# Performance work log

Hardware: AMD Instinct MI355X
Metric: run time of the kernel (lower is better)

The kernel has to match this reference:

```python
import jax, jax.numpy as jnp
import numpy as np

B, S, D, K = 4, 2048, 1024, 8

def setup_inputs() -> dict:
    key = jax.random.key(0)
    k1, k2, k3 = jax.random.split(key, 3)
    hidden_states = jax.random.normal(k1, (B, S, D), dtype=jnp.float32)
    # scaled so scores ~ O(1) and exp() does not overflow
    W_phi = jax.random.normal(k2, (D, D), dtype=jnp.float32) * 0.005
    W_psi = jax.random.normal(k3, (D, D), dtype=jnp.float32) * 0.005
    return {"hidden_states": hidden_states, "W_phi": W_phi, "W_psi": W_psi, "k": K}

def reference(hidden_states, W_phi, W_psi, k):
    b, s, d = hidden_states.shape
    k = min(k, s)
    # nn.Linear(bias=False): y = x @ W.T
    phi_h = hidden_states @ W_phi.T            # [b,s,d]
    psi_h = hidden_states @ W_psi.T            # [b,s,d]
    scores = jnp.einsum('bsd,btd->bst', phi_h, psi_h)  # [b,s,s]
    affinity = jnp.exp(scores)
    topk_values, topk_indices = jax.lax.top_k(affinity, k)   # [b,s,k]
    norm_sum = topk_values.sum(axis=-1, keepdims=True) + 1e-8
    normalized_weights = topk_values / norm_sum
    batch_offset = (jnp.arange(b) * s)[:, None, None]        # [b,1,1]
    src_local = jnp.arange(s)[None, :, None]                 # [1,s,1]
    src_global = jnp.broadcast_to(batch_offset + src_local, (b, s, k))
    dst_global = batch_offset + topk_indices
    mask = (topk_indices != src_local).reshape(-1)           # drop self-loops
    # eager boolean compaction (data-dependent size, like the torch module)
    src_final = src_global.reshape(-1)[mask]
    dst_final = dst_global.reshape(-1)[mask]
    weights_final = normalized_weights.reshape(-1)[mask]
    if src_final.size == 0:
        all_nodes = jnp.arange(b * s)
        return jnp.stack([all_nodes, all_nodes], axis=0), jnp.ones(b * s, dtype=jnp.float32)
    edge_index = jnp.stack([src_final, dst_final], axis=0)
    return edge_index, weights_final
```

## Files before the change

kernel.cpp:

```cpp
#include <hip/hip_runtime.h>
#include <cmath>

#define SEQ 2048
#define DDIM 1024
#define NROWS 8192
#define KSEL 8
#define IMAXC 0x7fffffff

typedef __attribute__((ext_vector_type(8))) short bf16x8;
typedef __attribute__((ext_vector_type(4))) float f32x4;
typedef __attribute__((ext_vector_type(4))) double f64x4;

__device__ __forceinline__ unsigned short f2bf(float f) {
  unsigned u = __builtin_bit_cast(unsigned, f);
  u = (u + 0x7fffu + ((u >> 16) & 1u)) >> 16;
  return (unsigned short)u;
}
__device__ __forceinline__ float bf2f(unsigned short h) {
  unsigned u = ((unsigned)h) << 16;
  return __builtin_bit_cast(float, u);
}
__device__ __forceinline__ unsigned pkbf(float a, float b) {
  unsigned r;
  asm("v_cvt_pk_bf16_f32 %0, %1, %2" : "=v"(r) : "v"(a), "v"(b));
  return r;
}
__device__ __forceinline__ void dmap(int sel, int lg, int lr, int rg,
                                     int& ri, int& ci) {
  switch (sel) {
    case 0:  ri = (lg << 2) + rg; ci = lr; break;
    case 1:  ri = lg + (rg << 2); ci = lr; break;
    case 2:  ri = lr; ci = (lg << 2) + rg; break;
    default: ri = lr; ci = lg + (rg << 2); break;
  }
}

__global__ void kprobe(int* __restrict__ sel) {
  const int lane = threadIdx.x;
  const int lr = lane & 15, lg = lane >> 4;
  const double a = (double)(4 * lr + lg + 1);
  const double b = (double)(9 * lr + 5 * lg + 2);
  f64x4 d = (f64x4){0.0, 0.0, 0.0, 0.0};
  d = __builtin_amdgcn_mfma_f64_16x16x4f64(a, b, d, 0, 0, 0);
  int my = 4;
  for (int s = 3; s >= 0; --s) {
    bool ok = true;
    for (int rg = 0; rg < 4; ++rg) {
      int ri, ci;
      dmap(s, lg, lr, rg, ri, ci);
      double e = 0.0;
      for (int k = 0; k < 4; ++k)
        e += (double)(4 * ri + k + 1) * (double)(9 * ci + 5 * k + 2);
      ok = ok && (d[rg] == e);
    }
    if (__all(ok)) my = s;
  }
  if (lane == 0) sel[0] = my;
}

__global__ __launch_bounds__(256, 2)
void k0_mfma(const float* __restrict__ A, const float* __restrict__ B,
             float* __restrict__ C, const int* __restrict__ selp) {
  const int sel = selp[0];
  if (sel >= 4) return;
  __shared__ float As[32][72];
  __shared__ float Bs[32][72];
  const int tid = threadIdx.x;
  const int lane = tid & 63, w = tid >> 6;
  const int wr = w >> 1, wc = w & 1;
  const int lr = lane & 15, lg = lane >> 4;
  const int brow = blockIdx.y << 6, bcol = blockIdx.x << 6;
  const int kr = tid >> 3, c4 = (tid & 7) << 2;

  f64x4 acc[2][2];
#pragma unroll
  for (int mi = 0; mi < 2; ++mi)
#pragma unroll
    for (int nj = 0; nj < 2; ++nj)
      acc[mi][nj] = (f64x4){0.0, 0.0, 0.0, 0.0};

  const float* Ap = &A[(size_t)kr * DDIM + brow + c4];
  const float* Bp = &B[(size_t)kr * DDIM + bcol + c4];
  float4 pa0 = *reinterpret_cast<const float4*>(Ap);
  float4 pa1 = *reinterpret_cast<const float4*>(Ap + 32);
  float4 pb0 = *reinterpret_cast<const float4*>(Bp);
  float4 pb1 = *reinterpret_cast<const float4*>(Bp + 32);

  for (int k0 = 0; k0 < DDIM; k0 += 32) {
    __syncthreads();
    *reinterpret_cast<float4*>(&As[kr][c4]) = pa0;
    *reinterpret_cast<float4*>(&As[kr][c4 + 32]) = pa1;
    *reinterpret_cast<float4*>(&Bs[kr][c4]) = pb0;
    *reinterpret_cast<float4*>(&Bs[kr][c4 + 32]) = pb1;
    __syncthreads();
    if (k0 + 32 < DDIM) {
      const size_t nk = (size_t)(k0 + 32) * DDIM;
      pa0 = *reinterpret_cast<const float4*>(Ap + nk);
      pa1 = *reinterpret_cast<const float4*>(Ap + nk + 32);
      pb0 = *reinterpret_cast<const float4*>(Bp + nk);
      pb1 = *reinterpret_cast<const float4*>(Bp + nk + 32);
    }
#pragma unroll
    for (int kp = 0; kp < 8; ++kp) {
      const int ka = (kp << 2) + lg;
      double a[2], b[2];
#pragma unroll
      for (int mi = 0; mi < 2; ++mi)
        a[mi] = (double)As[ka][(wr << 5) + (mi << 4) + lr];
#pragma unroll
      for (int nj = 0; nj < 2; ++nj)
        b[nj] = (double)Bs[ka][(wc << 5) + (nj << 4) + lr];
#pragma unroll
      for (int mi = 0; mi < 2; ++mi)
#pragma unroll
        for (int nj = 0; nj < 2; ++nj)
          acc[mi][nj] = __builtin_amdgcn_mfma_f64_16x16x4f64(
              a[mi], b[nj], acc[mi][nj], 0, 0, 0);
    }
  }
#pragma unroll
  for (int mi = 0; mi < 2; ++mi)
#pragma unroll
    for (int nj = 0; nj < 2; ++nj)
#pragma unroll
      for (int rg = 0; rg < 4; ++rg) {
        int ri, ci;
        dmap(sel, lg, lr, rg, ri, ci);
        C[(size_t)(brow + (wr << 5) + (mi << 4) + ri) * DDIM +
          bcol + (wc << 5) + (nj << 4) + ci] = (float)acc[mi][nj][rg];
      }
}

__global__ __launch_bounds__(256)
void k0_repair(const float* __restrict__ A, const float* __restrict__ B,
               float* __restrict__ C, const int* __restrict__ selp) {
  if (selp[0] < 4) return;
  __shared__ __align__(16) float As[32][68];
  __shared__ __align__(16) float Bs[32][68];
  const int tid = threadIdx.x;
  const int tx = tid & 15, ty = tid >> 4;
  const int brow = blockIdx.y << 6;
  const int bcol = blockIdx.x << 6;
  double acc[4][4] = {};
  for (int k0 = 0; k0 < DDIM; k0 += 32) {
#pragma unroll
    for (int i = 0; i < 2; ++i) {
      const int f = tid + (i << 8);
      const int r = f >> 4;
      const int c4 = (f & 15) << 2;
      *reinterpret_cast<float4*>(&As[r][c4]) =
          *reinterpret_cast<const float4*>(&A[(size_t)(k0 + r) * DDIM + brow + c4]);
      *reinterpret_cast<float4*>(&Bs[r][c4]) =
          *reinterpret_cast<const float4*>(&B[(size_t)(k0 + r) * DDIM + bcol + c4]);
    }
    __syncthreads();
#pragma unroll
    for (int kk = 0; kk < 32; ++kk) {
      const float4 a = *reinterpret_cast<const float4*>(&As[kk][ty << 2]);
      const float4 b = *reinterpret_cast<const float4*>(&Bs[kk][tx << 2]);
      const double ad[4] = {a.x, a.y, a.z, a.w};
      const double bd[4] = {b.x, b.y, b.z, b.w};
#pragma unroll
      for (int i = 0; i < 4; ++i)
#pragma unroll
        for (int j = 0; j < 4; ++j)
          acc[i][j] = fma(ad[i], bd[j], acc[i][j]);
    }
    __syncthreads();
  }
#pragma unroll
  for (int i = 0; i < 4; ++i) {
    float4 v = make_float4((float)acc[i][0], (float)acc[i][1],
                           (float)acc[i][2], (float)acc[i][3]);
    *reinterpret_cast<float4*>(
        &C[(size_t)(brow + (ty << 2) + i) * DDIM + bcol + (tx << 2)]) = v;
  }
}

#define K1_STAGE(bi)                                              \
  do {                                                            \
    As[bi][akh + 0][ar] = pa0.x; As[bi][akh + 1][ar] = pa0.y;     \
    As[bi][akh + 2][ar] = pa0.z; As[bi][akh + 3][ar] = pa0.w;     \
    As[bi][akh + 4][ar] = pa1.x; As[bi][akh + 5][ar] = pa1.y;     \
    As[bi][akh + 6][ar] = pa1.z; As[bi][akh + 7][ar] = pa1.w;     \
    *reinterpret_cast<float4*>(&Bs[bi][bk][bc4]) = pb0;           \
    *reinterpret_cast<float4*>(&Bs[bi][bk][bc4 + 64]) = pb1;      \
  } while (0)

__global__ __launch_bounds__(256, 2)
void k1_mfma(const float* __restrict__ A, const float* __restrict__ B,
             float* __restrict__ C, const int* __restrict__ selp) {
  const int sel = selp[0];
  if (sel >= 4) return;
  __shared__ float As[2][16][144];
  __shared__ float Bs[2][16][144];
  const int tid = threadIdx.x;
  const int lin = blockIdx.y * 8 + blockIdx.x;
  const int nlin = (lin & 7) * 64 + (lin >> 3);
  const int brow = (nlin >> 3) << 7;
  const int bcol = (nlin & 7) << 7;
  const int lane = tid & 63, w = tid >> 6;
  const int wr = w >> 1, wc = w & 1;
  const int lr = lane & 15, lg = lane >> 4;
  const int ar = tid >> 1, akh = (tid & 1) << 3;
  const int bk = tid >> 4, bc4 = (tid & 15) << 2;

  f64x4 acc[4][4];
#pragma unroll
  for (int mi = 0; mi < 4; ++mi)
#pragma unroll
    for (int nj = 0; nj < 4; ++nj)
      acc[mi][nj] = (f64x4){0.0, 0.0, 0.0, 0.0};

  const float* Ap = &A[(size_t)(brow + ar) * DDIM + akh];
  const float* Bp = &B[(size_t)bk * DDIM + bcol + bc4];

  float4 pa0 = *reinterpret_cast<const float4*>(Ap);
  float4 pa1 = *reinterpret_cast<const float4*>(Ap + 4);
  float4 pb0 = *reinterpret_cast<const float4*>(Bp);
  float4 pb1 = *reinterpret_cast<const float4*>(Bp + 64);
  K1_STAGE(0);
  pa0 = *reinterpret_cast<const float4*>(Ap + 16);
  pa1 = *reinterpret_cast<const float4*>(Ap + 20);
  pb0 = *reinterpret_cast<const float4*>(Bp + (size_t)16 * DDIM);
  pb1 = *reinterpret_cast<const float4*>(Bp + (size_t)16 * DDIM + 64);

  for (int t = 0; t < 64; ++t) {
    __syncthreads();
    const int cur = t & 1;
    if (t < 63) {
      K1_STAGE(cur ^ 1);
      if (t < 62) {
        const size_t ko = (size_t)(t + 2) << 4;
        pa0 = *reinterpret_cast<const float4*>(Ap + ko);
        pa1 = *reinterpret_cast<const float4*>(Ap + ko + 4);
        pb0 = *reinterpret_cast<const float4*>(Bp + ko * DDIM);
        pb1 = *reinterpret_cast<const float4*>(Bp + ko * DDIM + 64);
      }
    }
#pragma unroll
    for (int kp = 0; kp < 4; ++kp) {
      const int ka = (kp << 2) + lg;
      double a[4], b[4];
#pragma unroll
      for (int mi = 0; mi < 4; ++mi)
        a[mi] = (double)As[cur][ka][(wr << 6) + (mi << 4) + lr];
#pragma unroll
      for (int nj = 0; nj < 4; ++nj)
        b[nj] = (double)Bs[cur][ka][(wc << 6) + (nj << 4) + lr];
#pragma unroll
      for (int mi = 0; mi < 4; ++mi)
#pragma unroll
        for (int nj = 0; nj < 4; ++nj)
          acc[mi][nj] = __builtin_amdgcn_mfma_f64_16x16x4f64(
              a[mi], b[nj], acc[mi][nj], 0, 0, 0);
    }
  }
#pragma unroll
  for (int mi = 0; mi < 4; ++mi)
#pragma unroll
    for (int nj = 0; nj < 4; ++nj)
#pragma unroll
      for (int rg = 0; rg < 4; ++rg) {
        int ri, ci;
        dmap(sel, lg, lr, rg, ri, ci);
        C[(size_t)(brow + (wr << 6) + (mi << 4) + ri) * DDIM +
          bcol + (wc << 6) + (nj << 4) + ci] = (float)acc[mi][nj][rg];
      }
}

__global__ __launch_bounds__(256, 2)
void k1_repair(const float* __restrict__ A, const float* __restrict__ B,
               float* __restrict__ C, const int* __restrict__ selp) {
  if (selp[0] < 4) return;
  __shared__ double As[128][17];
  __shared__ double Bs[16][130];
  const int tid = threadIdx.x;
  const int lin = blockIdx.y * 8 + blockIdx.x;
  const int nlin = (lin & 7) * 64 + (lin >> 3);
  const int brow = (nlin >> 3) << 7;
  const int bcol = (nlin & 7) << 7;
  const int tx = tid & 15, ty = tid >> 4;
  const int ar = tid >> 1, aks = (tid & 1) << 3;
  const int bk = tid >> 4, btx = tid & 15;

  double acc[8][8];
#pragma unroll
  for (int i = 0; i < 8; ++i)
#pragma unroll
    for (int j = 0; j < 8; ++j) acc[i][j] = 0.0;

  const float* Aptr = &A[(size_t)(brow + ar) * DDIM + aks];
  const float* Bptr = &B[(size_t)bk * DDIM + bcol + (btx << 1)];

  float4 pa0, pa1;
  float2 pb[4];
  pa0 = *reinterpret_cast<const float4*>(Aptr);
  pa1 = *reinterpret_cast<const float4*>(Aptr + 4);
#pragma unroll
  for (int w = 0; w < 4; ++w)
    pb[w] = *reinterpret_cast<const float2*>(Bptr + (w << 5));

  for (int k0 = 0; k0 < DDIM; k0 += 16) {
    __syncthreads();
    As[ar][aks + 0] = (double)pa0.x; As[ar][aks + 1] = (double)pa0.y;
    As[ar][aks + 2] = (double)pa0.z; As[ar][aks + 3] = (double)pa0.w;
    As[ar][aks + 4] = (double)pa1.x; As[ar][aks + 5] = (double)pa1.y;
    As[ar][aks + 6] = (double)pa1.z; As[ar][aks + 7] = (double)pa1.w;
#pragma unroll
    for (int w = 0; w < 4; ++w) {
      Bs[bk][(btx << 1) + (w << 5) + 0] = (double)pb[w].x;
      Bs[bk][(btx << 1) + (w << 5) + 1] = (double)pb[w].y;
    }
    __syncthreads();
    if (k0 + 16 < DDIM) {
      pa0 = *reinterpret_cast<const float4*>(Aptr + k0 + 16);
      pa1 = *reinterpret_cast<const float4*>(Aptr + k0 + 20);
#pragma unroll
      for (int w = 0; w < 4; ++w)
        pb[w] = *reinterpret_cast<const float2*>(
            Bptr + (size_t)(k0 + 16) * DDIM + (w << 5));
    }
#pragma unroll 8
    for (int kk = 0; kk < 16; ++kk) {
      double a[8];
      double2 b[4];
#pragma unroll
      for (int i = 0; i < 8; ++i) a[i] = As[(ty << 3) + i][kk];
#pragma unroll
      for (int jj = 0; jj < 4; ++jj)
        b[jj] = *reinterpret_cast<const double2*>(&Bs[kk][(tx << 1) + (jj << 5)]);
#pragma unroll
      for (int i = 0; i < 8; ++i) {
#pragma unroll
        for (int jj = 0; jj < 4; ++jj) {
          acc[i][(jj << 1) + 0] = fma(a[i], b[jj].x, acc[i][(jj << 1) + 0]);
          acc[i][(jj << 1) + 1] = fma(a[i], b[jj].y, acc[i][(jj << 1) + 1]);
        }
      }
    }
  }
#pragma unroll
  for (int i = 0; i < 8; ++i) {
    float* crow = &C[(size_t)(brow + (ty << 3) + i) * DDIM + bcol + (tx << 1)];
#pragma unroll
    for (int jj = 0; jj < 4; ++jj) {
      float2 v = make_float2((float)acc[i][(jj << 1)],
                             (float)acc[i][(jj << 1) + 1]);
      *reinterpret_cast<float2*>(crow + (jj << 5)) = v;
    }
  }
}

__global__ __launch_bounds__(512, 1)
void k2_mfma(const float* __restrict__ T, const float* __restrict__ H,
             unsigned short* __restrict__ cand_v,
             unsigned char* __restrict__ cand_i) {
  __shared__ union {
    unsigned short stage[2][256 * 64];
    float Sl[64][264];
    struct {
      float mv[512][8];
      unsigned char mi[512][8];
    } mg;
  } u;
  const int tid = threadIdx.x;
  const int lane = tid & 63;
  const int w = tid >> 6;
  const int wr = w >> 2, wc = w & 3;
  const int lr = lane & 15, lg = lane >> 4;
  const int z = blockIdx.z;
  const int bx = blockIdx.x;
  const int brow = blockIdx.y << 8, bcol = bx << 8;
  const int row0g = z * SEQ + brow;
  const int col0g = z * SEQ + bcol;

  f32x4 acc[8][4];
#pragma unroll
  for (int mi = 0; mi < 8; ++mi)
#pragma unroll
    for (int nj = 0; nj < 4; ++nj)
      acc[mi][nj] = (f32x4){0.f, 0.f, 0.f, 0.f};

  for (int k0 = 0; k0 < DDIM; k0 += 64) {
    __syncthreads();
#pragma unroll
    for (int q = 0; q < 4; ++q) {
      const int c = (q << 9) + tid;
      const int row = c >> 3, slot = c & 7;
      const int gs = slot ^ (row & 7);
      {
        const float* s = &T[(size_t)(row0g + row) * DDIM + k0 + (gs << 3)];
        const float4 f0 = *reinterpret_cast<const float4*>(s);
        const float4 f1 = *reinterpret_cast<const float4*>(s + 4);
        uint4 o;
        o.x = pkbf(f0.x, f0.y); o.y = pkbf(f0.z, f0.w);
        o.z = pkbf(f1.x, f1.y); o.w = pkbf(f1.z, f1.w);
        *reinterpret_cast<uint4*>(&u.stage[0][c << 3]) = o;
      }
      {
        const float* s = &H[(size_t)(col0g + row) * DDIM + k0 + (gs << 3)];
        const float4 f0 = *reinterpret_cast<const float4*>(s);
        const float4 f1 = *reinterpret_cast<const float4*>(s + 4);
        uint4 o;
        o.x = pkbf(f0.x, f0.y); o.y = pkbf(f0.z, f0.w);
        o.z = pkbf(f1.x, f1.y); o.w = pkbf(f1.z, f1.w);
        *reinterpret_cast<uint4*>(&u.stage[1][c << 3]) = o;
      }
    }
    __syncthreads();
#pragma unroll
    for (int kh = 0; kh < 2; ++kh) {
      const int sl = (kh << 2) + lg;
      bf16x8 bfv[4];
#pragma unroll
      for (int nj = 0; nj < 4; ++nj) {
        const int rb = (wc << 6) + (nj << 4) + lr;
        bfv[nj] = *reinterpret_cast<const bf16x8*>(
            &u.stage[1][(rb << 6) + ((sl ^ (rb & 7)) << 3)]);
      }
#pragma unroll
      for (int mi = 0; mi < 8; ++mi) {
        const int ra = (wr << 7) + (mi << 4) + lr;
        const bf16x8 af = *reinterpret_cast<const bf16x8*>(
            &u.stage[0][(ra << 6) + ((sl ^ (ra & 7)) << 3)]);
#pragma unroll
        for (int nj = 0; nj < 4; ++nj)
          acc[mi][nj] = __builtin_amdgcn_mfma_f32_16x16x32_bf16(
              af, bfv[nj], acc[mi][nj], 0, 0, 0);
      }
    }
  }

  const int srow = tid >> 3;
  const int qd = tid & 7;
#pragma unroll
  for (int p = 0; p < 4; ++p) {
    __syncthreads();
    if (wr == (p >> 1)) {
      const int mib = (p & 1) << 2;
#pragma unroll
      for (int mi2 = 0; mi2 < 4; ++mi2)
#pragma unroll
        for (int nj = 0; nj < 4; ++nj)
#pragma unroll
          for (int rg = 0; rg < 4; ++rg)
            u.Sl[(mi2 << 4) + (lg << 2) + rg][(wc << 6) + (nj << 4) + lr] =
                acc[mib + mi2][nj][rg];
    }
    __syncthreads();
    float v[KSEL];
    int ci[KSEL];
#pragma unroll
    for (int s = 0; s < KSEL; ++s) { v[s] = -3.0e38f; ci[s] = 0; }
    const int c0 = qd << 5;
    for (int c = 0; c < 32; ++c) {
      const float x = u.Sl[srow][c0 + c];
      if (x > v[KSEL - 1]) {
        float pv = x; int pc = c0 + c;
#pragma unroll
        for (int s = 0; s < KSEL; ++s) {
          if (x > v[s]) {
            const float tv = v[s]; const int tc = ci[s];
            v[s] = pv; ci[s] = pc; pv = tv; pc = tc;
          }
        }
      }
    }
    __syncthreads();
#pragma unroll
    for (int s = 0; s < KSEL; ++s) {
      u.mg.mv[tid][s] = v[s];
      u.mg.mi[tid][s] = (unsigned char)ci[s];
    }
    __syncthreads();
    if (qd == 0) {
      float fv[KSEL];
      int fi[KSEL];
#pragma unroll
      for (int s = 0; s < KSEL; ++s) { fv[s] = -3.0e38f; fi[s] = 0; }
#pragma unroll
      for (int t = 0; t < 8; ++t) {
#pragma unroll
        for (int s = 0; s < KSEL; ++s) {
          const float x = u.mg.mv[tid + t][s];
          const int idx = u.mg.mi[tid + t][s];
          if (x > fv[KSEL - 1]) {
            float pv = x; int pc = idx;
#pragma unroll
            for (int s2 = 0; s2 < KSEL; ++s2) {
              if (x > fv[s2]) {
                const float tv = fv[s2]; const int tc = fi[s2];
                fv[s2] = pv; fi[s2] = pc; pv = tv; pc = tc;
              }
            }
          }
        }
      }
      const size_t base =
          (size_t)(row0g + (p << 6) + srow) * 64 + ((size_t)bx << 3);
#pragma unroll
      for (int s = 0; s < KSEL; ++s) {
        cand_v[base + s] = f2bf(fv[s]);
        cand_i[base + s] = (unsigned char)fi[s];
      }
    }
  }
}

__global__ __launch_bounds__(256)
void kr_rescore(const float* __restrict__ T, const float* __restrict__ H,
                const unsigned short* __restrict__ cand_v,
                const unsigned char* __restrict__ cand_i,
                int* __restrict__ topi, float* __restrict__ topw,
                int* __restrict__ cnt) {
  const int tid = threadIdx.x, lane = tid & 63, w = tid >> 6;
  const int r = blockIdx.x * 4 + w;
  const int b = r >> 11, iloc = r & (SEQ - 1);

  const size_t cbase = (size_t)r * 64;
  float v0 = bf2f(cand_v[cbase + lane]);
  int i0 = ((lane >> 3) << 8) + cand_i[cbase + lane];
  int keep = 0;
  for (int rnd = 0; rnd < 16; ++rnd) {
    float m = v0;
#pragma unroll
    for (int off = 32; off >= 1; off >>= 1) m = fmaxf(m, __shfl_xor(m, off));
    const unsigned long long bm = __ballot(v0 == m);
    const int owner = __ffsll(bm) - 1;
    const int oi = __shfl(i0, owner);
    if (lane == owner) v0 = -3.0e38f;
    if (lane == rnd) keep = oi;
  }

  const float* Trow = T + (size_t)r * DDIM;
  float4 t4[4];
#pragma unroll
  for (int q = 0; q < 4; ++q)
    t4[q] = *reinterpret_cast<const float4*>(&Trow[(q << 8) + (lane << 2)]);

  float t8v[KSEL];
  int t8i[KSEL];
#pragma unroll
  for (int p = 0; p < KSEL; ++p) { t8v[p] = -1.0f; t8i[p] = IMAXC; }

  for (int c = 0; c < 16; ++c) {
    const int j = __shfl(keep, c);
    const float* Hrow = H + ((size_t)(b << 11) + j) * DDIM;
    double s = 0.0;
#pragma unroll
    for (int q = 0; q < 4; ++q) {
      const float4 h = *reinterpret_cast<const float4*>(&Hrow[(q << 8) + (lane << 2)]);
      s = fma((double)t4[q].x, (double)h.x, s);
      s = fma((double)t4[q].y, (double)h.y, s);
      s = fma((double)t4[q].z, (double)h.z, s);
      s = fma((double)t4[q].w, (double)h.w, s);
    }
#pragma unroll
    for (int off = 1; off < 64; off <<= 1) s += __shfl_xor(s, off);
    const float aff = expf((float)s);
    const bool g7 = (aff > t8v[KSEL - 1]) ||
                    (aff == t8v[KSEL - 1] && j < t8i[KSEL - 1]);
    if (g7) {
      float pv = aff; int pi = j;
#pragma unroll
      for (int p = 0; p < KSEL; ++p) {
        const bool g = (aff > t8v[p]) || (aff == t8v[p] && j < t8i[p]);
        if (g) {
          const float tv = t8v[p]; const int ti = t8i[p];
          t8v[p] = pv; t8i[p] = pi; pv = tv; pi = ti;
        }
      }
    }
  }
  if (lane == 0) {
    float sum = 0.0f;
#pragma unroll
    for (int p = 0; p < KSEL; ++p) sum += t8v[p];
    sum += 1e-8f;
    int c8 = KSEL;
#pragma unroll
    for (int p = 0; p < KSEL; ++p)
      if (t8i[p] == iloc) --c8;
    cnt[r] = c8;
#pragma unroll
    for (int p = 0; p < KSEL; ++p) {
      topi[(size_t)r * KSEL + p] = t8i[p];
      topw[(size_t)r * KSEL + p] = t8v[p] / sum;
    }
  }
}

__global__ __launch_bounds__(1024)
void k4_scan(const int* __restrict__ cnt, int* __restrict__ off) {
  __shared__ int part[1024];
  const int t = threadIdx.x;
  int loc[8];
  int s = 0;
#pragma unroll
  for (int i = 0; i < 8; ++i) { loc[i] = s; s += cnt[t * 8 + i]; }
  part[t] = s;
  __syncthreads();
  for (int d = 1; d < 1024; d <<= 1) {
    const int add = (t >= d) ? part[t - d] : 0;
    __syncthreads();
    part[t] += add;
    __syncthreads();
  }
  const int base = (t == 0) ? 0 : part[t - 1];
#pragma unroll
  for (int i = 0; i < 8; ++i) off[t * 8 + i] = base + loc[i];
}

__global__ __launch_bounds__(256)
void k5_emit(const int* __restrict__ topi, const float* __restrict__ topw,
             const int* __restrict__ off, float* __restrict__ out, int E) {
  const int r = blockIdx.x * 256 + threadIdx.x;
  if (r >= NROWS) return;
  const int o = off[r];
  const int sloc = r & (SEQ - 1);
  const int bbase = r & ~(SEQ - 1);
  int e = 0;
#pragma unroll
  for (int p = 0; p < KSEL; ++p) {
    const int id = topi[(size_t)r * KSEL + p];
    const float w = topw[(size_t)r * KSEL + p];
    if (id != sloc) {
      const int pos = o + e;
      if (pos < E) {
        out[pos] = (float)r;
        out[(size_t)E + pos] = (float)(bbase + id);
        out[2 * (size_t)E + pos] = w;
      }
      ++e;
    }
  }
}

extern "C" void kernel_launch(void* const* d_in, const int* in_sizes, int n_in,
                              void* d_out, int out_size, void* d_ws,
                              size_t ws_size, hipStream_t stream) {
  const float* H = (const float*)d_in[0];
  const float* Wphi = (const float*)d_in[1];
  const float* Wpsi = (const float*)d_in[2];
  float* out = (float*)d_out;
  const int E = out_size / 3;

  char* base = (char*)d_ws;
  float* T = (float*)base;
  char* regionX = base + 33554432;
  float* Wc = (float*)regionX;
  unsigned short* cand_v = (unsigned short*)regionX;
  unsigned char* cand_i = (unsigned char*)(regionX + 2097152);
  char* pp = regionX + 4194304;
  int* topi = (int*)pp;  pp += 262144;
  float* topw = (float*)pp; pp += 262144;
  int* cnt = (int*)pp;   pp += 32768;
  int* off = (int*)pp;   pp += 32768;
  int* sel = (int*)pp;

  kprobe<<<dim3(1), 64, 0, stream>>>(sel);
  k0_mfma<<<dim3(16, 16), 256, 0, stream>>>(Wphi, Wpsi, Wc, sel);
  k0_repair<<<dim3(16, 16), 256, 0, stream>>>(Wphi, Wpsi, Wc, sel);
  k1_mfma<<<dim3(8, 64), 256, 0, stream>>>(H, Wc, T, sel);
  k1_repair<<<dim3(8, 64), 256, 0, stream>>>(H, Wc, T, sel);
  k2_mfma<<<dim3(8, 8, 4), 512, 0, stream>>>(T, H, cand_v, cand_i);
  kr_rescore<<<dim3(NROWS / 4), 256, 0, stream>>>(T, H, cand_v, cand_i,
                                                  topi, topw, cnt);
  k4_scan<<<dim3(1), 1024, 0, stream>>>(cnt, off);
  k5_emit<<<dim3(NROWS / 256), 256, 0, stream>>>(topi, topw, off, out, E);
}
```

Before: 592.1 us.

## Double-buffer LDS staging in k0 and k2 GEMMs and raise MFMA wave priority

New measurement: 563.0 us. 1.05x faster.

```diff
diff --git a/kernel.cpp b/kernel.cpp
--- a/kernel.cpp
+++ b/kernel.cpp
@@ -58,13 +58,21 @@
   if (lane == 0) sel[0] = my;
 }
 
+#define K0_STAGE(bi)                                        \
+  do {                                                      \
+    *reinterpret_cast<float4*>(&As[bi][kr][c4]) = pa0;      \
+    *reinterpret_cast<float4*>(&As[bi][kr][c4 + 32]) = pa1; \
+    *reinterpret_cast<float4*>(&Bs[bi][kr][c4]) = pb0;      \
+    *reinterpret_cast<float4*>(&Bs[bi][kr][c4 + 32]) = pb1; \
+  } while (0)
+
 __global__ __launch_bounds__(256, 2)
 void k0_mfma(const float* __restrict__ A, const float* __restrict__ B,
              float* __restrict__ C, const int* __restrict__ selp) {
   const int sel = selp[0];
   if (sel >= 4) return;
-  __shared__ float As[32][72];
-  __shared__ float Bs[32][72];
+  __shared__ float As[2][32][72];
+  __shared__ float Bs[2][32][72];
   const int tid = threadIdx.x;
   const int lane = tid & 63, w = tid >> 6;
   const int wr = w >> 1, wc = w & 1;
@@ -85,31 +93,39 @@
   float4 pa1 = *reinterpret_cast<const float4*>(Ap + 32);
   float4 pb0 = *reinterpret_cast<const float4*>(Bp);
   float4 pb1 = *reinterpret_cast<const float4*>(Bp + 32);
-
-  for (int k0 = 0; k0 < DDIM; k0 += 32) {
-    __syncthreads();
-    *reinterpret_cast<float4*>(&As[kr][c4]) = pa0;
-    *reinterpret_cast<float4*>(&As[kr][c4 + 32]) = pa1;
-    *reinterpret_cast<float4*>(&Bs[kr][c4]) = pb0;
-    *reinterpret_cast<float4*>(&Bs[kr][c4 + 32]) = pb1;
-    __syncthreads();
-    if (k0 + 32 < DDIM) {
-      const size_t nk = (size_t)(k0 + 32) * DDIM;
-      pa0 = *reinterpret_cast<const float4*>(Ap + nk);
-      pa1 = *reinterpret_cast<const float4*>(Ap + nk + 32);
-      pb0 = *reinterpret_cast<const float4*>(Bp + nk);
-      pb1 = *reinterpret_cast<const float4*>(Bp + nk + 32);
-    }
+  K0_STAGE(0);
+  {
+    const size_t nk = (size_t)32 * DDIM;
+    pa0 = *reinterpret_cast<const float4*>(Ap + nk);
+    pa1 = *reinterpret_cast<const float4*>(Ap + nk + 32);
+    pb0 = *reinterpret_cast<const float4*>(Bp + nk);
+    pb1 = *reinterpret_cast<const float4*>(Bp + nk + 32);
+  }
+
+  for (int t = 0; t < 32; ++t) {
+    __syncthreads();
+    const int cur = t & 1;
+    if (t < 31) {
+      K0_STAGE(cur ^ 1);
+      if (t < 30) {
+        const size_t nk = (size_t)(t + 2) * 32 * DDIM;
+        pa0 = *reinterpret_cast<const float4*>(Ap + nk);
+        pa1 = *reinterpret_cast<const float4*>(Ap + nk + 32);
+        pb0 = *reinterpret_cast<const float4*>(Bp + nk);
+        pb1 = *reinterpret_cast<const float4*>(Bp + nk + 32);
+      }
+    }
+    __builtin_amdgcn_s_setprio(1);
 #pragma unroll
     for (int kp = 0; kp < 8; ++kp) {
       const int ka = (kp << 2) + lg;
       double a[2], b[2];
 #pragma unroll
       for (int mi = 0; mi < 2; ++mi)
-        a[mi] = (double)As[ka][(wr << 5) + (mi << 4) + lr];
+        a[mi] = (double)As[cur][ka][(wr << 5) + (mi << 4) + lr];
 #pragma unroll
       for (int nj = 0; nj < 2; ++nj)
-        b[nj] = (double)Bs[ka][(wc << 5) + (nj << 4) + lr];
+        b[nj] = (double)Bs[cur][ka][(wc << 5) + (nj << 4) + lr];
 #pragma unroll
       for (int mi = 0; mi < 2; ++mi)
 #pragma unroll
@@ -117,6 +133,7 @@
           acc[mi][nj] = __builtin_amdgcn_mfma_f64_16x16x4f64(
               a[mi], b[nj], acc[mi][nj], 0, 0, 0);
     }
+    __builtin_amdgcn_s_setprio(0);
   }
 #pragma unroll
   for (int mi = 0; mi < 2; ++mi)
@@ -238,6 +255,7 @@
         pb1 = *reinterpret_cast<const float4*>(Bp + ko * DDIM + 64);
       }
     }
+    __builtin_amdgcn_s_setprio(1);
 #pragma unroll
     for (int kp = 0; kp < 4; ++kp) {
       const int ka = (kp << 2) + lg;
@@ -255,6 +273,7 @@
           acc[mi][nj] = __builtin_amdgcn_mfma_f64_16x16x4f64(
               a[mi], b[nj], acc[mi][nj], 0, 0, 0);
     }
+    __builtin_amdgcn_s_setprio(0);
   }
 #pragma unroll
   for (int mi = 0; mi < 4; ++mi)
@@ -352,12 +371,48 @@
   }
 }
 
+#define K2_LOAD(koff)                                                         \
+  do {                                                                        \
+    _Pragma("unroll")                                                         \
+    for (int q = 0; q < 4; ++q) {                                             \
+      const int c = (q << 9) + tid;                                           \
+      const int row = c >> 3;                                                 \
+      const int gs = (c & 7) ^ (row & 7);                                     \
+      const float* sT = &T[(size_t)(row0g + row) * DDIM + (koff) + (gs << 3)];\
+      rT[2 * q] = *reinterpret_cast<const float4*>(sT);                       \
+      rT[2 * q + 1] = *reinterpret_cast<const float4*>(sT + 4);               \
+      const float* sH = &H[(size_t)(col0g + row) * DDIM + (koff) + (gs << 3)];\
+      rH[2 * q] = *reinterpret_cast<const float4*>(sH);                       \
+      rH[2 * q + 1] = *reinterpret_cast<const float4*>(sH + 4);               \
+    }                                                                         \
+  } while (0)
+
+#define K2_STAGE(bi)                                                          \
+  do {                                                                        \
+    _Pragma("unroll")                                                         \
+    for (int q = 0; q < 4; ++q) {                                             \
+      const int c = (q << 9) + tid;                                           \
+      uint4 o;                                                                \
+      o.x = pkbf(rT[2 * q].x, rT[2 * q].y);                                   \
+      o.y = pkbf(rT[2 * q].z, rT[2 * q].w);                                   \
+      o.z = pkbf(rT[2 * q + 1].x, rT[2 * q + 1].y);                           \
+      o.w = pkbf(rT[2 * q + 1].z, rT[2 * q + 1].w);                           \
+      *reinterpret_cast<uint4*>(&u.stage[bi][0][c << 3]) = o;                 \
+      uint4 o2;                                                               \
+      o2.x = pkbf(rH[2 * q].x, rH[2 * q].y);                                  \
+      o2.y = pkbf(rH[2 * q].z, rH[2 * q].w);                                  \
+      o2.z = pkbf(rH[2 * q + 1].x, rH[2 * q + 1].y);                          \
+      o2.w = pkbf(rH[2 * q + 1].z, rH[2 * q + 1].w);                          \
+      *reinterpret_cast<uint4*>(&u.stage[bi][1][c << 3]) = o2;                \
+    }                                                                         \
+  } while (0)
+
 __global__ __launch_bounds__(512, 1)
 void k2_mfma(const float* __restrict__ T, const float* __restrict__ H,
              unsigned short* __restrict__ cand_v,
              unsigned char* __restrict__ cand_i) {
   __shared__ union {
-    unsigned short stage[2][256 * 64];
+    unsigned short stage[2][2][256 * 64];
     float Sl[64][264];
     struct {
       float mv[512][8];
@@ -382,33 +437,18 @@
     for (int nj = 0; nj < 4; ++nj)
       acc[mi][nj] = (f32x4){0.f, 0.f, 0.f, 0.f};
 
-  for (int k0 = 0; k0 < DDIM; k0 += 64) {
-    __syncthreads();
-#pragma unroll
-    for (int q = 0; q < 4; ++q) {
-      const int c = (q << 9) + tid;
-      const int row = c >> 3, slot = c & 7;
-      const int gs = slot ^ (row & 7);
-      {
-        const float* s = &T[(size_t)(row0g + row) * DDIM + k0 + (gs << 3)];
-        const float4 f0 = *reinterpret_cast<const float4*>(s);
-        const float4 f1 = *reinterpret_cast<const float4*>(s + 4);
-        uint4 o;
-        o.x = pkbf(f0.x, f0.y); o.y = pkbf(f0.z, f0.w);
-        o.z = pkbf(f1.x, f1.y); o.w = pkbf(f1.z, f1.w);
-        *reinterpret_cast<uint4*>(&u.stage[0][c << 3]) = o;
-      }
-      {
-        const float* s = &H[(size_t)(col0g + row) * DDIM + k0 + (gs << 3)];
-        const float4 f0 = *reinterpret_cast<const float4*>(s);
-        const float4 f1 = *reinterpret_cast<const float4*>(s + 4);
-        uint4 o;
-        o.x = pkbf(f0.x, f0.y); o.y = pkbf(f0.z, f0.w);
-        o.z = pkbf(f1.x, f1.y); o.w = pkbf(f1.z, f1.w);
-        *reinterpret_cast<uint4*>(&u.stage[1][c << 3]) = o;
-      }
-    }
-    __syncthreads();
+  float4 rT[8], rH[8];
+  K2_LOAD(0);
+  K2_STAGE(0);
+  K2_LOAD(64);
+
+  for (int t = 0; t < 16; ++t) {
+    __syncthreads();
+    const int cur = t & 1;
+    if (t < 15) {
+      K2_STAGE(cur ^ 1);
+      if (t < 14) K2_LOAD((t + 2) << 6);
+    }
 #pragma unroll
     for (int kh = 0; kh < 2; ++kh) {
       const int sl = (kh << 2) + lg;
@@ -417,13 +457,13 @@
       for (int nj = 0; nj < 4; ++nj) {
         const int rb = (wc << 6) + (nj << 4) + lr;
         bfv[nj] = *reinterpret_cast<const bf16x8*>(
-            &u.stage[1][(rb << 6) + ((sl ^ (rb & 7)) << 3)]);
+            &u.stage[cur][1][(rb << 6) + ((sl ^ (rb & 7)) << 3)]);
       }
 #pragma unroll
       for (int mi = 0; mi < 8; ++mi) {
         const int ra = (wr << 7) + (mi << 4) + lr;
         const bf16x8 af = *reinterpret_cast<const bf16x8*>(
-            &u.stage[0][(ra << 6) + ((sl ^ (ra & 7)) << 3)]);
+            &u.stage[cur][0][(ra << 6) + ((sl ^ (ra & 7)) << 3)]);
 #pragma unroll
         for (int nj = 0; nj < 4; ++nj)
           acc[mi][nj] = __builtin_amdgcn_mfma_f32_16x16x32_bf16(
@@ -480,11 +520,11 @@
 #pragma unroll
       for (int s = 0; s < KSEL; ++s) { fv[s] = -3.0e38f; fi[s] = 0; }
 #pragma unroll
-      for (int t = 0; t < 8; ++t) {
+      for (int t2 = 0; t2 < 8; ++t2) {
 #pragma unroll
         for (int s = 0; s < KSEL; ++s) {
-          const float x = u.mg.mv[tid + t][s];
-          const int idx = u.mg.mi[tid + t][s];
+          const float x = u.mg.mv[tid + t2][s];
+          const int idx = u.mg.mi[tid + t2][s];
           if (x > fv[KSEL - 1]) {
             float pv = x; int pc = idx;
 #pragma unroll
```
